# Optimization experiments

Measured on AMD Instinct MI355X. Metric: run time of the kernel, lower is better.

Reference implementation:

```python
import jax, jax.numpy as jnp
import numpy as np
import math

HID = 1024; HEADS = 8; DH = 128; CS = 200; MAXPOS = 512; K = 15; EXP = 2; MULT = 4
SCALE = DH ** -0.5
CEXP = HID * EXP  # 2048 depthwise channels


def _ln(x, g, b, eps=1e-5):
    m = jnp.mean(x, axis=-1, keepdims=True)
    v = jnp.var(x, axis=-1, keepdims=True)
    return (x - m) * jax.lax.rsqrt(v + eps) * g + b


def _ff(x, ng, nb, w1, b1, w2, b2):
    h = jax.nn.silu(_ln(x, ng, nb) @ w1 + b1)
    return h @ w2 + b2


def _attn(x, dists, ng, nb, wq, wkv, pos_emb, wo, bo):
    B, N, _ = x.shape
    x = _ln(x, ng, nb)
    nblk = math.ceil(N / CS)
    rem = N % CS
    if rem:
        x = jnp.pad(x, ((0, 0), (0, CS - rem), (0, 0)))

    def heads(t):  # [B, M*C, H*Dh] -> [B, M, H, C, Dh]
        return t.reshape(B, nblk, CS, HEADS, DH).transpose(0, 1, 3, 2, 4)

    q = heads(x @ wq)
    k, v = jnp.split(x @ wkv, 2, axis=-1)
    k, v = heads(k), heads(v)
    rel = pos_emb[dists]  # [C, C, Dh] Shaw relative position embeddings
    pos_attn = jnp.einsum('bmhcd,crd->bmhcr', q, rel) * SCALE
    if rem:
        mask = jnp.ones((CS, CS), bool).at[:rem, :rem].set(False)
        big_neg = -jnp.finfo(pos_attn.dtype).max
        pos_attn = pos_attn.at[:, -1].set(jnp.where(mask, big_neg, pos_attn[:, -1]))
    scores = jnp.einsum('bmhcd,bmhrd->bmhcr', q, k) * SCALE + pos_attn
    p = jax.nn.softmax(scores, axis=-1)
    o = jnp.einsum('bmhcr,bmhrd->bmhcd', p, v)
    o = o.transpose(0, 1, 3, 2, 4).reshape(B, nblk * CS, HEADS * DH)[:, :N]
    return o @ wo + bo


def _conv(x, ng, nb, pw1_w, pw1_b, dw_w, bn_g, bn_b, bn_m, bn_v, pw2_w, pw2_b):
    h = _ln(x, ng, nb) @ pw1_w + pw1_b            # [B, N, 2*CEXP] pointwise conv1
    a, gate = jnp.split(h, 2, axis=-1)
    h = (a * jax.nn.sigmoid(gate)).transpose(0, 2, 1)  # GLU -> [B, CEXP, N]
    pad = (K - 1) // 2
    h = jax.lax.conv_general_dilated(h, dw_w[:, None, :], (1,), [(pad, pad)],
                                     feature_group_count=CEXP,
                                     dimension_numbers=('NCH', 'OIH', 'NCH'))
    # BatchNorm1d in eval mode (running stats)
    h = (h - bn_m[:, None]) * jax.lax.rsqrt(bn_v[:, None] + 1e-5) * bn_g[:, None] + bn_b[:, None]
    h = jax.nn.silu(h).transpose(0, 2, 1)
    return h @ pw2_w + pw2_b


def setup_inputs() -> dict:
    ks = iter(jax.random.split(jax.random.key(0), 16))
    def nrm(shape, s=0.05):
        return jax.random.normal(next(ks), shape, dtype=jnp.float32) * s
    return {
        'x': jax.random.normal(next(ks), (8, 2000, HID), dtype=jnp.float32),
        'attention_dists': jax.random.randint(next(ks), (CS, CS), 0, 2 * MAXPOS + 1),
        'ff1_ng': jnp.ones((HID,)), 'ff1_nb': jnp.zeros((HID,)),
        'ff1_w1': nrm((HID, HID * MULT)), 'ff1_b1': jnp.zeros((HID * MULT,)),
        'ff1_w2': nrm((HID * MULT, HID)), 'ff1_b2': jnp.zeros((HID,)),
        'attn_ng': jnp.ones((HID,)), 'attn_nb': jnp.zeros((HID,)),
        'wq': nrm((HID, HEADS * DH)), 'wkv': nrm((HID, 2 * HEADS * DH)),
        'pos_emb': nrm((2 * MAXPOS + 1, DH)),
        'wo': nrm((HEADS * DH, HID)), 'bo': jnp.zeros((HID,)),
        'conv_ng': jnp.ones((HID,)), 'conv_nb': jnp.zeros((HID,)),
        'pw1_w': nrm((HID, 2 * CEXP)), 'pw1_b': jnp.zeros((2 * CEXP,)),
        'dw_w': nrm((CEXP, K)),
        'bn_g': jnp.ones((CEXP,)), 'bn_b': jnp.zeros((CEXP,)),
        'bn_m': jnp.zeros((CEXP,)), 'bn_v': jnp.ones((CEXP,)),
        'pw2_w': nrm((CEXP, HID)), 'pw2_b': jnp.zeros((HID,)),
        'ff2_ng': jnp.ones((HID,)), 'ff2_nb': jnp.zeros((HID,)),
        'ff2_w1': nrm((HID, HID * MULT)), 'ff2_b1': jnp.zeros((HID * MULT,)),
        'ff2_w2': nrm((HID * MULT, HID)), 'ff2_b2': jnp.zeros((HID,)),
        'post_g': jnp.ones((HID,)), 'post_b': jnp.zeros((HID,)),
    }


def reference(x, attention_dists, ff1_ng, ff1_nb, ff1_w1, ff1_b1, ff1_w2, ff1_b2,
              attn_ng, attn_nb, wq, wkv, pos_emb, wo, bo,
              conv_ng, conv_nb, pw1_w, pw1_b, dw_w, bn_g, bn_b, bn_m, bn_v, pw2_w, pw2_b,
              ff2_ng, ff2_nb, ff2_w1, ff2_b1, ff2_w2, ff2_b2, post_g, post_b):
    x = x + 0.5 * _ff(x, ff1_ng, ff1_nb, ff1_w1, ff1_b1, ff1_w2, ff1_b2)
    x = x + _attn(x, attention_dists, attn_ng, attn_nb, wq, wkv, pos_emb, wo, bo)
    x = x + _conv(x, conv_ng, conv_nb, pw1_w, pw1_b, dw_w, bn_g, bn_b, bn_m, bn_v, pw2_w, pw2_b)
    x = x + 0.5 * _ff(x, ff2_ng, ff2_nb, ff2_w1, ff2_b1, ff2_w2, ff2_b2)
    return _ln(x, post_g, post_b)
```

## Files before the change

kernel.cpp:

```cpp
#include <hip/hip_runtime.h>
#include <hip/hip_bf16.h>
#include <stdint.h>

using bf16 = __hip_bfloat16;
typedef __bf16 bf16x8v __attribute__((ext_vector_type(8)));
typedef float f32x4 __attribute__((ext_vector_type(4)));

#define MFMA16(a,b,c) __builtin_amdgcn_mfma_f32_16x16x32_bf16((a),(b),(c),0,0,0)

__device__ __forceinline__ float tof(bf16 h){ return __bfloat162float(h); }
__device__ __forceinline__ bf16 tob(float f){ return __float2bfloat16(f); }

__device__ __forceinline__ void gll16(const void* g, void* l) {
    __builtin_amdgcn_global_load_lds((const __attribute__((address_space(1))) void*)g,
                                     (__attribute__((address_space(3))) void*)l, 16, 0, 0);
}

__global__ __launch_bounds__(256)
void zero_k(uint4* __restrict__ p, size_t n)
{
    size_t i = (size_t)blockIdx.x * 256 + threadIdx.x;
    size_t st = (size_t)gridDim.x * 256;
    uint4 z = make_uint4(0u, 0u, 0u, 0u);
    for (; i < n; i += st) p[i] = z;
}

__global__ __launch_bounds__(256)
void transpose_cast(const float* __restrict__ in, bf16* __restrict__ out, int R, int C)
{
    __shared__ float t[32][33];
    int bx = blockIdx.x * 32, by = blockIdx.y * 32;
    int tx = threadIdx.x & 31, ty = threadIdx.x >> 5;
#pragma unroll
    for (int i = 0; i < 4; ++i)
        t[ty + i*8][tx] = in[(size_t)(by + ty + i*8) * C + bx + tx];
    __syncthreads();
#pragma unroll
    for (int i = 0; i < 4; ++i)
        out[(size_t)(bx + ty + i*8) * R + by + tx] = tob(t[tx][ty + i*8]);
}

template<bool OUT32>
__global__ __launch_bounds__(256)
void ln_k(const float* __restrict__ x, const float* __restrict__ g,
          const float* __restrict__ b, void* __restrict__ out)
{
    int row = blockIdx.x, tid = threadIdx.x;
    const float4 v = ((const float4*)(x + (size_t)row*1024))[tid];
    float s = v.x + v.y + v.z + v.w;
    float q = v.x*v.x + v.y*v.y + v.z*v.z + v.w*v.w;
#pragma unroll
    for (int m = 1; m < 64; m <<= 1) { s += __shfl_xor(s, m); q += __shfl_xor(q, m); }
    __shared__ float red[8];
    if ((tid & 63) == 0) { red[tid>>6] = s; red[4 + (tid>>6)] = q; }
    __syncthreads();
    float ts = red[0]+red[1]+red[2]+red[3];
    float tq = red[4]+red[5]+red[6]+red[7];
    float mean = ts * (1.f/1024.f);
    float var  = tq * (1.f/1024.f) - mean*mean;
    float rs = rsqrtf(var + 1e-5f);
    const float4 gv = ((const float4*)g)[tid];
    const float4 bv = ((const float4*)b)[tid];
    float o0 = (v.x-mean)*rs*gv.x + bv.x;
    float o1 = (v.y-mean)*rs*gv.y + bv.y;
    float o2 = (v.z-mean)*rs*gv.z + bv.z;
    float o3 = (v.w-mean)*rs*gv.w + bv.w;
    if (OUT32) {
        ((float4*)out)[(size_t)row*256 + tid] = make_float4(o0,o1,o2,o3);
    } else {
        bf16 tmp[4] = { tob(o0), tob(o1), tob(o2), tob(o3) };
        ((uint2*)out)[(size_t)row*256 + tid] = *(const uint2*)tmp;
    }
}

template<int EP>
__global__ __launch_bounds__(256, 2)
void gemm_bt(const bf16* __restrict__ A, const bf16* __restrict__ BT,
             int M, int N, int K, int lda,
             const float* __restrict__ bias, const float* resid, float alpha,
             void* o0, void* o1, void* o2)
{
    (void)M;
    __shared__ bf16 sA[2][4096];
    __shared__ bf16 sB[2][4096];
    const int tid = threadIdx.x;
    const int lane = tid & 63, wid = tid >> 6;
    const int wm = wid >> 1, wn = wid & 1;
    const int bn0 = blockIdx.x * 128, bm0 = blockIdx.y * 128;
    const int fr = lane & 15, fq = lane >> 4;
    const int nk = K >> 5;

    f32x4 acc[4][4];
    const f32x4 vzero = {0.f, 0.f, 0.f, 0.f};
#pragma unroll
    for (int i = 0; i < 4; ++i)
#pragma unroll
        for (int j = 0; j < 4; ++j) acc[i][j] = vzero;

    const bf16* Abase = A + (size_t)bm0 * lda;
    const bf16* Bbase = BT + (size_t)bn0 * K;

    auto stage = [&](int kb, int buf) {
#pragma unroll
        for (int rd = 0; rd < 2; ++rd) {
            int s = rd*256 + tid;
            int r = s >> 2, ko = (s & 3) * 8;
            gll16(Abase + (size_t)r*lda + kb*32 + ko, &sA[buf][s*8]);
            gll16(Bbase + (size_t)r*K   + kb*32 + ko, &sB[buf][s*8]);
        }
    };

    stage(0, 0);
    for (int kb = 0; kb < nk; ++kb) {
        __syncthreads();
        if (kb + 1 < nk) stage(kb+1, (kb+1) & 1);
        const bf16* sa = sA[kb & 1];
        const bf16* sb = sB[kb & 1];
        bf16x8v af[4], bfv[4];
#pragma unroll
        for (int mi = 0; mi < 4; ++mi)
            af[mi] = *(const bf16x8v*)(sa + (wm*64 + mi*16 + fr)*32 + fq*8);
#pragma unroll
        for (int ni = 0; ni < 4; ++ni)
            bfv[ni] = *(const bf16x8v*)(sb + (wn*64 + ni*16 + fr)*32 + fq*8);
#pragma unroll
        for (int mi = 0; mi < 4; ++mi)
#pragma unroll
            for (int ni = 0; ni < 4; ++ni)
                acc[mi][ni] = MFMA16(af[mi], bfv[ni], acc[mi][ni]);
    }

#pragma unroll
    for (int mi = 0; mi < 4; ++mi)
#pragma unroll
    for (int ni = 0; ni < 4; ++ni)
#pragma unroll
    for (int r = 0; r < 4; ++r) {
        int row = bm0 + wm*64 + mi*16 + fq*4 + r;
        int col = bn0 + wn*64 + ni*16 + fr;
        float v = acc[mi][ni][r];
        if (EP == 0) {
            v += bias[col];
            v = v * (1.f / (1.f + __expf(-v)));
            ((bf16*)o0)[(size_t)row * N + col] = tob(v);
        } else if (EP == 1) {
            v += bias[col];
            ((bf16*)o0)[(size_t)row * N + col] = tob(v);
        } else if (EP == 2) {
            float o = resid[(size_t)row * N + col] + alpha * (v + bias[col]);
            ((float*)o0)[(size_t)row * N + col] = o;
        } else {
            int sec = col >> 10, hh = (col >> 7) & 7, d = col & 127;
            int blk = (row / 200) * 8 + hh, c = row % 200;
            if (sec == 0)      ((bf16*)o0)[((size_t)blk*208 + c)*128 + d] = tob(v * 0.08838834764831845f);
            else if (sec == 1) ((bf16*)o1)[((size_t)blk*208 + c)*128 + d] = tob(v);
            else               ((bf16*)o2)[((size_t)blk*128 + d)*224 + c] = tob(v);
        }
    }
}

__global__ __launch_bounds__(64)
void pos_kernel(const bf16* __restrict__ qb, const float* __restrict__ pe,
                const int* __restrict__ dists, bf16* __restrict__ pbuf)
{
    const int c = blockIdx.y, mt = blockIdx.x;
    const int lane = threadIdx.x;
    const int fr = lane & 15, fq = lane >> 4;
    bf16x8v qa[4][4];
#pragma unroll
    for (int sub = 0; sub < 4; ++sub)
#pragma unroll
        for (int kk = 0; kk < 4; ++kk)
            qa[sub][kk] = *(const bf16x8v*)(qb + ((size_t)(mt*64 + sub*16 + fr)*208 + c)*128 + kk*32 + fq*8);

    for (int rt = 0; rt < 13; ++rt) {
        int r = rt*16 + fr;
        int pidx = (r < 200) ? dists[c*200 + r] : 0;
        bf16x8v bv[4];
#pragma unroll
        for (int kk = 0; kk < 4; ++kk) {
            const float* pp = pe + (size_t)pidx*128 + kk*32 + fq*8;
            f32x4 lo = *(const f32x4*)pp;
            f32x4 hi = *(const f32x4*)(pp + 4);
            bf16x8v t;
#pragma unroll
            for (int j = 0; j < 4; ++j) { t[j] = (__bf16)lo[j]; t[4+j] = (__bf16)hi[j]; }
            bv[kk] = t;
        }
#pragma unroll
        for (int sub = 0; sub < 4; ++sub) {
            f32x4 a = {0.f,0.f,0.f,0.f};
#pragma unroll
            for (int kk = 0; kk < 4; ++kk) a = MFMA16(qa[sub][kk], bv[kk], a);
            int bmh = mt*64 + sub*16 + fq*4;
#pragma unroll
            for (int g = 0; g < 4; ++g)
                pbuf[((size_t)c*640 + bmh + g)*208 + r] = tob(a[g]);
        }
    }
}

__global__ __launch_bounds__(256, 2)
void attn_core(const bf16* __restrict__ qb, const bf16* __restrict__ kb,
               const bf16* __restrict__ vt, const bf16* __restrict__ pb,
               bf16* __restrict__ ob)
{
    __shared__ bf16 P[4][16][224];
    const int blk = blockIdx.x;
    const int tid = threadIdx.x, lane = tid & 63, w = tid >> 6;
    const int fr = lane & 15, fq = lane >> 4;
    const size_t qkbase = (size_t)blk * 208 * 128;
    const size_t vbase  = (size_t)blk * 128 * 224;

    for (int qc = w; qc < 13; qc += 4) {
        bf16x8v qa[4];
#pragma unroll
        for (int kk = 0; kk < 4; ++kk)
            qa[kk] = *(const bf16x8v*)(qb + qkbase + (size_t)(qc*16 + fr)*128 + kk*32 + fq*8);

        f32x4 s[13];
#pragma unroll
        for (int rt = 0; rt < 13; ++rt) {
            f32x4 a = {0.f,0.f,0.f,0.f};
#pragma unroll
            for (int kk = 0; kk < 4; ++kk) {
                bf16x8v kf = *(const bf16x8v*)(kb + qkbase + (size_t)(rt*16 + fr)*128 + kk*32 + fq*8);
                a = MFMA16(qa[kk], kf, a);
            }
            s[rt] = a;
        }
#pragma unroll
        for (int rt = 0; rt < 13; ++rt) {
            int r = rt*16 + fr;
#pragma unroll
            for (int g = 0; g < 4; ++g) {
                int c = qc*16 + fq*4 + g;
                float v = s[rt][g];
                if (c < 200) v += tof(pb[((size_t)c*640 + blk)*208 + r]);
                if (r >= 200) v = -1e30f;
                s[rt][g] = v;
            }
        }
        float mx[4] = {-3e38f,-3e38f,-3e38f,-3e38f};
#pragma unroll
        for (int rt = 0; rt < 13; ++rt)
#pragma unroll
            for (int g = 0; g < 4; ++g) mx[g] = fmaxf(mx[g], s[rt][g]);
#pragma unroll
        for (int m = 1; m < 16; m <<= 1)
#pragma unroll
            for (int g = 0; g < 4; ++g) mx[g] = fmaxf(mx[g], __shfl_xor(mx[g], m));
        float sm[4] = {0.f,0.f,0.f,0.f};
#pragma unroll
        for (int rt = 0; rt < 13; ++rt)
#pragma unroll
            for (int g = 0; g < 4; ++g) {
                float pv = __expf(s[rt][g] - mx[g]);
                s[rt][g] = pv; sm[g] += pv;
            }
#pragma unroll
        for (int m = 1; m < 16; m <<= 1)
#pragma unroll
            for (int g = 0; g < 4; ++g) sm[g] += __shfl_xor(sm[g], m);
        float inv[4];
#pragma unroll
        for (int g = 0; g < 4; ++g) inv[g] = 1.f / sm[g];
#pragma unroll
        for (int rt = 0; rt < 13; ++rt)
#pragma unroll
            for (int g = 0; g < 4; ++g)
                P[w][fq*4 + g][rt*16 + fr] = tob(s[rt][g] * inv[g]);
#pragma unroll
        for (int g = 0; g < 4; ++g) P[w][fq*4 + g][208 + fr] = tob(0.f);
        asm volatile("s_waitcnt lgkmcnt(0)" ::: "memory");
        __builtin_amdgcn_sched_barrier(0);

        bf16x8v pa[7];
#pragma unroll
        for (int kt = 0; kt < 7; ++kt)
            pa[kt] = *(const bf16x8v*)(&P[w][fr][kt*32 + fq*8]);
#pragma unroll
        for (int nt = 0; nt < 8; ++nt) {
            f32x4 o = {0.f,0.f,0.f,0.f};
#pragma unroll
            for (int kt = 0; kt < 7; ++kt) {
                bf16x8v vf = *(const bf16x8v*)(vt + vbase + (size_t)(nt*16 + fr)*224 + kt*32 + fq*8);
                o = MFMA16(pa[kt], vf, o);
            }
            int d = nt*16 + fr;
#pragma unroll
            for (int g = 0; g < 4; ++g) {
                int c = qc*16 + fq*4 + g;
                if (c < 200)
                    ob[((size_t)(blk >> 3)*200 + c)*1024 + (blk & 7)*128 + d] = tob(o[g]);
            }
        }
    }
}

__global__ __launch_bounds__(256)
void glu_k(bf16* __restrict__ h)
{
    size_t idx = (size_t)blockIdx.x*256 + threadIdx.x;
    size_t row = idx >> 8; int c0 = (int)(idx & 255) * 8;
    bf16* pa = h + row*4096 + c0;
    const bf16* pg = h + row*4096 + 2048 + c0;
    union { uint4 u; bf16 hh[8]; } a, g, o;
    a.u = *(const uint4*)pa; g.u = *(const uint4*)pg;
#pragma unroll
    for (int j = 0; j < 8; ++j) {
        float av = tof(a.hh[j]), gv = tof(g.hh[j]);
        o.hh[j] = tob(av * (1.f / (1.f + __expf(-gv))));
    }
    *(uint4*)pa = o.u;
}

__global__ __launch_bounds__(256)
void dwconv(const bf16* __restrict__ h, const float* __restrict__ dw,
            const float* __restrict__ bng, const float* __restrict__ bnb,
            const float* __restrict__ bnm, const float* __restrict__ bnv,
            bf16* __restrict__ out)
{
    int ch = blockIdx.x*256 + threadIdx.x;
    int b  = blockIdx.z;
    int n0 = blockIdx.y * 125;
    float wgt[15];
#pragma unroll
    for (int i = 0; i < 15; ++i) wgt[i] = dw[ch*15 + i];
    float sc = bng[ch] * rsqrtf(bnv[ch] + 1e-5f);
    float sh = bnb[ch] - bnm[ch]*sc;
    const size_t rowbase = (size_t)b*2000;
    float win[15];
#pragma unroll
    for (int i = 0; i < 15; ++i) {
        int nn = n0 - 7 + i;
        win[i] = (nn >= 0 && nn < 2000) ? tof(h[(rowbase + nn)*4096 + ch]) : 0.f;
    }
    for (int j = 0; j < 125; ++j) {
        int n = n0 + j;
        float a = 0.f;
#pragma unroll
        for (int i = 0; i < 15; ++i) a += win[i]*wgt[i];
        float y = a*sc + sh;
        y = y * (1.f / (1.f + __expf(-y)));
        out[(rowbase + n)*4096 + ch] = tob(y);
#pragma unroll
        for (int i = 0; i < 14; ++i) win[i] = win[i+1];
        int nn = n + 8;
        win[14] = (nn < 2000) ? tof(h[(rowbase + nn)*4096 + ch]) : 0.f;
    }
}

extern "C" void kernel_launch(void* const* d_in, const int* in_sizes, int n_in,
                              void* d_out, int out_size, void* d_ws, size_t ws_size,
                              hipStream_t stream)
{
    (void)in_sizes; (void)n_in; (void)out_size; (void)ws_size;
    const float* x      = (const float*)d_in[0];
    const int*   dists  = (const int*)d_in[1];
    const float* ff1_ng = (const float*)d_in[2];
    const float* ff1_nb = (const float*)d_in[3];
    const float* ff1_w1 = (const float*)d_in[4];
    const float* ff1_b1 = (const float*)d_in[5];
    const float* ff1_w2 = (const float*)d_in[6];
    const float* ff1_b2 = (const float*)d_in[7];
    const float* attn_ng= (const float*)d_in[8];
    const float* attn_nb= (const float*)d_in[9];
    const float* wq     = (const float*)d_in[10];
    const float* wkv    = (const float*)d_in[11];
    const float* pos_emb= (const float*)d_in[12];
    const float* wo     = (const float*)d_in[13];
    const float* bo     = (const float*)d_in[14];
    const float* conv_ng= (const float*)d_in[15];
    const float* conv_nb= (const float*)d_in[16];
    const float* pw1_w  = (const float*)d_in[17];
    const float* pw1_b  = (const float*)d_in[18];
    const float* dw_w   = (const float*)d_in[19];
    const float* bn_g   = (const float*)d_in[20];
    const float* bn_b   = (const float*)d_in[21];
    const float* bn_m   = (const float*)d_in[22];
    const float* bn_v   = (const float*)d_in[23];
    const float* pw2_w  = (const float*)d_in[24];
    const float* pw2_b  = (const float*)d_in[25];
    const float* ff2_ng = (const float*)d_in[26];
    const float* ff2_nb = (const float*)d_in[27];
    const float* ff2_w1 = (const float*)d_in[28];
    const float* ff2_b1 = (const float*)d_in[29];
    const float* ff2_w2 = (const float*)d_in[30];
    const float* ff2_b2 = (const float*)d_in[31];
    const float* post_g = (const float*)d_in[32];
    const float* post_b = (const float*)d_in[33];

    float* xres = (float*)d_out;

    char* p = (char*)d_ws;
    bf16*  xn    = (bf16*)p;   p += 32768000;
    bf16* ff1w1T = (bf16*)p;   p += 8388608;
    bf16* ff1w2T = (bf16*)p;   p += 8388608;
    bf16* qkvT   = (bf16*)p;   p += 6291456;
    bf16* woT    = (bf16*)p;   p += 2097152;
    bf16* pw1T   = (bf16*)p;   p += 8388608;
    bf16* pw2T   = (bf16*)p;   p += 4194304;
    bf16* ff2w1T = (bf16*)p;   p += 8388608;
    bf16* ff2w2T = (bf16*)p;   p += 8388608;
    char* trans  = p;
    bf16* qbuf = (bf16*)trans;
    bf16* kbuf = qbuf + (size_t)640*208*128;
    bf16* vT   = kbuf + (size_t)640*208*128;
    bf16* posb = vT   + (size_t)640*128*224;
    bf16* hbuf = (bf16*)trans;

    transpose_cast<<<dim3(128, 32), 256, 0, stream>>>(ff1_w1, ff1w1T, 1024, 4096);
    transpose_cast<<<dim3(32, 128), 256, 0, stream>>>(ff1_w2, ff1w2T, 4096, 1024);
    transpose_cast<<<dim3(32, 32),  256, 0, stream>>>(wq, qkvT, 1024, 1024);
    transpose_cast<<<dim3(64, 32),  256, 0, stream>>>(wkv, qkvT + (size_t)1024*1024, 1024, 2048);
    transpose_cast<<<dim3(32, 32),  256, 0, stream>>>(wo, woT, 1024, 1024);
    transpose_cast<<<dim3(128, 32), 256, 0, stream>>>(pw1_w, pw1T, 1024, 4096);
    transpose_cast<<<dim3(32, 64),  256, 0, stream>>>(pw2_w, pw2T, 2048, 1024);
    transpose_cast<<<dim3(128, 32), 256, 0, stream>>>(ff2_w1, ff2w1T, 1024, 4096);
    transpose_cast<<<dim3(32, 128), 256, 0, stream>>>(ff2_w2, ff2w2T, 4096, 1024);

    ln_k<false><<<16000, 256, 0, stream>>>(x, ff1_ng, ff1_nb, xn);
    gemm_bt<0><<<dim3(32,125), 256, 0, stream>>>(xn, ff1w1T, 16000,4096,1024,1024,
                                                 ff1_b1, nullptr, 0.f, hbuf, nullptr, nullptr);
    gemm_bt<2><<<dim3(8,125), 256, 0, stream>>>(hbuf, ff1w2T, 16000,1024,4096,4096,
                                                ff1_b2, x, 0.5f, xres, nullptr, nullptr);

    ln_k<false><<<16000, 256, 0, stream>>>(xres, attn_ng, attn_nb, xn);
    zero_k<<<2048, 256, 0, stream>>>((uint4*)qbuf, (size_t)104857600/16);
    gemm_bt<3><<<dim3(24,125), 256, 0, stream>>>(xn, qkvT, 16000,3072,1024,1024,
                                                 nullptr, nullptr, 0.f, qbuf, kbuf, vT);
    pos_kernel<<<dim3(10,200), 64, 0, stream>>>(qbuf, pos_emb, dists, posb);
    attn_core<<<640, 256, 0, stream>>>(qbuf, kbuf, vT, posb, xn);
    gemm_bt<2><<<dim3(8,125), 256, 0, stream>>>(xn, woT, 16000,1024,1024,1024,
                                                bo, xres, 1.f, xres, nullptr, nullptr);

    ln_k<false><<<16000, 256, 0, stream>>>(xres, conv_ng, conv_nb, xn);
    gemm_bt<1><<<dim3(32,125), 256, 0, stream>>>(xn, pw1T, 16000,4096,1024,1024,
                                                 pw1_b, nullptr, 0.f, hbuf, nullptr, nullptr);
    glu_k<<<16000, 256, 0, stream>>>(hbuf);
    dwconv<<<dim3(8,16,8), 256, 0, stream>>>(hbuf, dw_w, bn_g, bn_b, bn_m, bn_v, hbuf + 2048);
    gemm_bt<2><<<dim3(8,125), 256, 0, stream>>>(hbuf + 2048, pw2T, 16000,1024,2048,4096,
                                                pw2_b, xres, 1.f, xres, nullptr, nullptr);

    ln_k<false><<<16000, 256, 0, stream>>>(xres, ff2_ng, ff2_nb, xn);
    gemm_bt<0><<<dim3(32,125), 256, 0, stream>>>(xn, ff2w1T, 16000,4096,1024,1024,
                                                 ff2_b1, nullptr, 0.f, hbuf, nullptr, nullptr);
    gemm_bt<2><<<dim3(8,125), 256, 0, stream>>>(hbuf, ff2w2T, 16000,1024,4096,4096,
                                                ff2_b2, xres, 0.5f, xres, nullptr, nullptr);

    ln_k<true><<<16000, 256, 0, stream>>>(xres, post_g, post_b, d_out);
}
```

Measured before the change: 2.009 ms.

## Zero only attention padding, pre-cast pos embeddings, split attention by query tile

Replaces the full 100MB zero-fill of the Q/K/V transit buffers with a kernel that zeroes only the padded rows and columns. Pos embeddings are cast to bf16 once, so pos_kernel loads bf16 directly instead of converting fp32 per use. attn_core now runs one 64-thread block per (head-block, query tile) and computes S transposed, so softmax reduces over only 2 shuffles and P writes and pos loads are vectorised. This trades the shared-memory-free parallelism inside a block for more, smaller blocks, and depends on the rest of the buffers being fully written by the QKV GEMM.

```diff
diff --git a/kernel.cpp b/kernel.cpp
--- a/kernel.cpp
+++ b/kernel.cpp
@@ -17,12 +17,31 @@
 }
 
 __global__ __launch_bounds__(256)
-void zero_k(uint4* __restrict__ p, size_t n)
-{
-    size_t i = (size_t)blockIdx.x * 256 + threadIdx.x;
-    size_t st = (size_t)gridDim.x * 256;
-    uint4 z = make_uint4(0u, 0u, 0u, 0u);
-    for (; i < n; i += st) p[i] = z;
+void pad_zero(bf16* __restrict__ q, bf16* __restrict__ k, bf16* __restrict__ v)
+{
+    int blk = blockIdx.x, t = threadIdx.x;
+    uint2 z = make_uint2(0u, 0u);
+    size_t qk = (size_t)blk * 208 * 128;
+    int r = 200 + (t >> 5), c = (t & 31) * 4;
+    *(uint2*)(q + qk + r*128 + c) = z;
+    *(uint2*)(k + qk + r*128 + c) = z;
+    size_t vb = (size_t)blk * 128 * 224;
+    int d = t >> 1, c0 = 200 + (t & 1) * 12;
+    *(uint2*)(v + vb + d*224 + c0)     = z;
+    *(uint2*)(v + vb + d*224 + c0 + 4) = z;
+    *(uint2*)(v + vb + d*224 + c0 + 8) = z;
+}
+
+__global__ __launch_bounds__(256)
+void cast_pe(const float* __restrict__ in, bf16* __restrict__ out, int n8)
+{
+    int i = blockIdx.x * 256 + threadIdx.x;
+    if (i >= n8) return;
+    f32x4 a = ((const f32x4*)in)[2*i], b = ((const f32x4*)in)[2*i + 1];
+    union { uint4 u; bf16 h[8]; } o;
+#pragma unroll
+    for (int j = 0; j < 4; ++j) { o.h[j] = tob(a[j]); o.h[4+j] = tob(b[j]); }
+    ((uint4*)out)[i] = o.u;
 }
 
 __global__ __launch_bounds__(256)
@@ -160,7 +179,7 @@
 }
 
 __global__ __launch_bounds__(64)
-void pos_kernel(const bf16* __restrict__ qb, const float* __restrict__ pe,
+void pos_kernel(const bf16* __restrict__ qb, const bf16* __restrict__ peb,
                 const int* __restrict__ dists, bf16* __restrict__ pbuf)
 {
     const int c = blockIdx.y, mt = blockIdx.x;
@@ -178,15 +197,8 @@
         int pidx = (r < 200) ? dists[c*200 + r] : 0;
         bf16x8v bv[4];
 #pragma unroll
-        for (int kk = 0; kk < 4; ++kk) {
-            const float* pp = pe + (size_t)pidx*128 + kk*32 + fq*8;
-            f32x4 lo = *(const f32x4*)pp;
-            f32x4 hi = *(const f32x4*)(pp + 4);
-            bf16x8v t;
-#pragma unroll
-            for (int j = 0; j < 4; ++j) { t[j] = (__bf16)lo[j]; t[4+j] = (__bf16)hi[j]; }
-            bv[kk] = t;
-        }
+        for (int kk = 0; kk < 4; ++kk)
+            bv[kk] = *(const bf16x8v*)(peb + (size_t)pidx*128 + kk*32 + fq*8);
 #pragma unroll
         for (int sub = 0; sub < 4; ++sub) {
             f32x4 a = {0.f,0.f,0.f,0.f};
@@ -200,100 +212,91 @@
     }
 }
 
-__global__ __launch_bounds__(256, 2)
+__global__ __launch_bounds__(64, 4)
 void attn_core(const bf16* __restrict__ qb, const bf16* __restrict__ kb,
                const bf16* __restrict__ vt, const bf16* __restrict__ pb,
                bf16* __restrict__ ob)
 {
-    __shared__ bf16 P[4][16][224];
-    const int blk = blockIdx.x;
-    const int tid = threadIdx.x, lane = tid & 63, w = tid >> 6;
+    __shared__ bf16 P[16][232];
+    const int blk = blockIdx.x, qc = blockIdx.y;
+    const int lane = threadIdx.x;
     const int fr = lane & 15, fq = lane >> 4;
     const size_t qkbase = (size_t)blk * 208 * 128;
     const size_t vbase  = (size_t)blk * 128 * 224;
-
-    for (int qc = w; qc < 13; qc += 4) {
-        bf16x8v qa[4];
-#pragma unroll
-        for (int kk = 0; kk < 4; ++kk)
-            qa[kk] = *(const bf16x8v*)(qb + qkbase + (size_t)(qc*16 + fr)*128 + kk*32 + fq*8);
-
-        f32x4 s[13];
-#pragma unroll
-        for (int rt = 0; rt < 13; ++rt) {
-            f32x4 a = {0.f,0.f,0.f,0.f};
-#pragma unroll
-            for (int kk = 0; kk < 4; ++kk) {
-                bf16x8v kf = *(const bf16x8v*)(kb + qkbase + (size_t)(rt*16 + fr)*128 + kk*32 + fq*8);
-                a = MFMA16(qa[kk], kf, a);
-            }
-            s[rt] = a;
-        }
-#pragma unroll
-        for (int rt = 0; rt < 13; ++rt) {
-            int r = rt*16 + fr;
-#pragma unroll
-            for (int g = 0; g < 4; ++g) {
-                int c = qc*16 + fq*4 + g;
-                float v = s[rt][g];
-                if (c < 200) v += tof(pb[((size_t)c*640 + blk)*208 + r]);
-                if (r >= 200) v = -1e30f;
-                s[rt][g] = v;
-            }
-        }
-        float mx[4] = {-3e38f,-3e38f,-3e38f,-3e38f};
-#pragma unroll
-        for (int rt = 0; rt < 13; ++rt)
-#pragma unroll
-            for (int g = 0; g < 4; ++g) mx[g] = fmaxf(mx[g], s[rt][g]);
-#pragma unroll
-        for (int m = 1; m < 16; m <<= 1)
-#pragma unroll
-            for (int g = 0; g < 4; ++g) mx[g] = fmaxf(mx[g], __shfl_xor(mx[g], m));
-        float sm[4] = {0.f,0.f,0.f,0.f};
-#pragma unroll
-        for (int rt = 0; rt < 13; ++rt)
-#pragma unroll
-            for (int g = 0; g < 4; ++g) {
-                float pv = __expf(s[rt][g] - mx[g]);
-                s[rt][g] = pv; sm[g] += pv;
-            }
-#pragma unroll
-        for (int m = 1; m < 16; m <<= 1)
-#pragma unroll
-            for (int g = 0; g < 4; ++g) sm[g] += __shfl_xor(sm[g], m);
-        float inv[4];
-#pragma unroll
-        for (int g = 0; g < 4; ++g) inv[g] = 1.f / sm[g];
-#pragma unroll
-        for (int rt = 0; rt < 13; ++rt)
+    const int c = qc*16 + fr;
+
+    bf16x8v qa[4];
+#pragma unroll
+    for (int kk = 0; kk < 4; ++kk)
+        qa[kk] = *(const bf16x8v*)(qb + qkbase + (size_t)(qc*16 + fr)*128 + kk*32 + fq*8);
+
+    f32x4 s[13];
+#pragma unroll
+    for (int rt = 0; rt < 13; ++rt) {
+        f32x4 a = {0.f,0.f,0.f,0.f};
+#pragma unroll
+        for (int kk = 0; kk < 4; ++kk) {
+            bf16x8v kf = *(const bf16x8v*)(kb + qkbase + (size_t)(rt*16 + fr)*128 + kk*32 + fq*8);
+            a = MFMA16(kf, qa[kk], a);
+        }
+        s[rt] = a;
+    }
+#pragma unroll
+    for (int rt = 0; rt < 13; ++rt) {
+        if (c < 200) {
+            union { uint2 u; bf16 h[4]; } pv;
+            pv.u = *(const uint2*)(pb + ((size_t)c*640 + blk)*208 + rt*16 + fq*4);
+#pragma unroll
+            for (int g = 0; g < 4; ++g) s[rt][g] += tof(pv.h[g]);
+        }
+        if (rt == 12 && fq >= 2) {
 #pragma unroll
             for (int g = 0; g < 4; ++g)
-                P[w][fq*4 + g][rt*16 + fr] = tob(s[rt][g] * inv[g]);
-#pragma unroll
-        for (int g = 0; g < 4; ++g) P[w][fq*4 + g][208 + fr] = tob(0.f);
-        asm volatile("s_waitcnt lgkmcnt(0)" ::: "memory");
-        __builtin_amdgcn_sched_barrier(0);
-
-        bf16x8v pa[7];
-#pragma unroll
-        for (int kt = 0; kt < 7; ++kt)
-            pa[kt] = *(const bf16x8v*)(&P[w][fr][kt*32 + fq*8]);
-#pragma unroll
-        for (int nt = 0; nt < 8; ++nt) {
-            f32x4 o = {0.f,0.f,0.f,0.f};
-#pragma unroll
-            for (int kt = 0; kt < 7; ++kt) {
-                bf16x8v vf = *(const bf16x8v*)(vt + vbase + (size_t)(nt*16 + fr)*224 + kt*32 + fq*8);
-                o = MFMA16(pa[kt], vf, o);
-            }
-            int d = nt*16 + fr;
-#pragma unroll
-            for (int g = 0; g < 4; ++g) {
-                int c = qc*16 + fq*4 + g;
-                if (c < 200)
-                    ob[((size_t)(blk >> 3)*200 + c)*1024 + (blk & 7)*128 + d] = tob(o[g]);
-            }
+                if (fq*4 + g >= 8) s[rt][g] = -1e30f;
+        }
+    }
+    float mx = -3e38f;
+#pragma unroll
+    for (int rt = 0; rt < 13; ++rt)
+#pragma unroll
+        for (int g = 0; g < 4; ++g) mx = fmaxf(mx, s[rt][g]);
+    mx = fmaxf(mx, __shfl_xor(mx, 16));
+    mx = fmaxf(mx, __shfl_xor(mx, 32));
+    float sm = 0.f;
+#pragma unroll
+    for (int rt = 0; rt < 13; ++rt)
+#pragma unroll
+        for (int g = 0; g < 4; ++g) { float pv = __expf(s[rt][g] - mx); s[rt][g] = pv; sm += pv; }
+    sm += __shfl_xor(sm, 16);
+    sm += __shfl_xor(sm, 32);
+    float inv = 1.f / sm;
+#pragma unroll
+    for (int rt = 0; rt < 13; ++rt) {
+        union { uint2 u; bf16 h[4]; } pw;
+#pragma unroll
+        for (int g = 0; g < 4; ++g) pw.h[g] = tob(s[rt][g] * inv);
+        *(uint2*)&P[fr][rt*16 + fq*4] = pw.u;
+    }
+    *(uint2*)&P[fr][208 + fq*4] = make_uint2(0u, 0u);
+
+    bf16x8v pa[7];
+#pragma unroll
+    for (int kt = 0; kt < 7; ++kt)
+        pa[kt] = *(const bf16x8v*)(&P[fr][kt*32 + fq*8]);
+#pragma unroll
+    for (int nt = 0; nt < 8; ++nt) {
+        f32x4 o = {0.f,0.f,0.f,0.f};
+#pragma unroll
+        for (int kt = 0; kt < 7; ++kt) {
+            bf16x8v vf = *(const bf16x8v*)(vt + vbase + (size_t)(nt*16 + fr)*224 + kt*32 + fq*8);
+            o = MFMA16(pa[kt], vf, o);
+        }
+        int d = nt*16 + fr;
+#pragma unroll
+        for (int g = 0; g < 4; ++g) {
+            int cc = qc*16 + fq*4 + g;
+            if (cc < 200)
+                ob[((size_t)(blk >> 3)*200 + cc)*1024 + (blk & 7)*128 + d] = tob(o[g]);
         }
     }
 }
@@ -403,6 +406,7 @@
     bf16* pw2T   = (bf16*)p;   p += 4194304;
     bf16* ff2w1T = (bf16*)p;   p += 8388608;
     bf16* ff2w2T = (bf16*)p;   p += 8388608;
+    bf16* peb    = (bf16*)p;   p += 262400;
     char* trans  = p;
     bf16* qbuf = (bf16*)trans;
     bf16* kbuf = qbuf + (size_t)640*208*128;
@@ -419,6 +423,7 @@
     transpose_cast<<<dim3(32, 64),  256, 0, stream>>>(pw2_w, pw2T, 2048, 1024);
     transpose_cast<<<dim3(128, 32), 256, 0, stream>>>(ff2_w1, ff2w1T, 1024, 4096);
     transpose_cast<<<dim3(32, 128), 256, 0, stream>>>(ff2_w2, ff2w2T, 4096, 1024);
+    cast_pe<<<65, 256, 0, stream>>>(pos_emb, peb, 16400);
 
     ln_k<false><<<16000, 256, 0, stream>>>(x, ff1_ng, ff1_nb, xn);
     gemm_bt<0><<<dim3(32,125), 256, 0, stream>>>(xn, ff1w1T, 16000,4096,1024,1024,
@@ -427,11 +432,11 @@
                                                 ff1_b2, x, 0.5f, xres, nullptr, nullptr);
 
     ln_k<false><<<16000, 256, 0, stream>>>(xres, attn_ng, attn_nb, xn);
-    zero_k<<<2048, 256, 0, stream>>>((uint4*)qbuf, (size_t)104857600/16);
+    pad_zero<<<640, 256, 0, stream>>>(qbuf, kbuf, vT);
     gemm_bt<3><<<dim3(24,125), 256, 0, stream>>>(xn, qkvT, 16000,3072,1024,1024,
                                                  nullptr, nullptr, 0.f, qbuf, kbuf, vT);
-    pos_kernel<<<dim3(10,200), 64, 0, stream>>>(qbuf, pos_emb, dists, posb);
-    attn_core<<<640, 256, 0, stream>>>(qbuf, kbuf, vT, posb, xn);
+    pos_kernel<<<dim3(10,200), 64, 0, stream>>>(qbuf, peb, dists, posb);
+    attn_core<<<dim3(640,13), 64, 0, stream>>>(qbuf, kbuf, vT, posb, xn);
     gemm_bt<2><<<dim3(8,125), 256, 0, stream>>>(xn, woT, 16000,1024,1024,1024,
                                                 bo, xres, 1.f, xres, nullptr, nullptr);
 
```

Result: faster. 1.877 ms (-6.6%).
